# Performance work log

Measured on AMD Instinct MI355X. Metric: run time of the kernel, lower is better.

Reference implementation:

```python
import jax, jax.numpy as jnp
import numpy as np

B, T, IN_DIM = 128, 512, 32
H = 256            # h_dim; bidirectional -> embedding_dim D = 2*H = 512
N_EMB = 1024
BETA = 0.25


def setup_inputs() -> dict:
    key = jax.random.key(0)
    ks = jax.random.split(key, 12)
    traj = jax.random.normal(ks[0], (B, T, IN_DIM), dtype=jnp.float32)
    # variable-length padding mask: ones up to length, zeros after
    lengths = jax.random.randint(ks[1], (B,), 1, T + 1)
    mask = (jnp.arange(T)[None, :] < lengths[:, None]).astype(jnp.int32)
    s_x = 1.0 / np.sqrt(H)
    def u(k, shape):
        return jax.random.uniform(k, shape, jnp.float32, -s_x, s_x)
    # PyTorch GRU param layout: W_ih [3H, in], W_hh [3H, H], biases [3H]
    Wx_f, Wh_f = u(ks[2], (3 * H, IN_DIM)), u(ks[3], (3 * H, H))
    bx_f, bh_f = u(ks[4], (3 * H,)), u(ks[5], (3 * H,))
    Wx_b, Wh_b = u(ks[6], (3 * H, IN_DIM)), u(ks[7], (3 * H, H))
    bx_b, bh_b = u(ks[8], (3 * H,)), u(ks[9], (3 * H,))
    # codebook: nn.Embedding(n_embeddings, D) with uniform(-1/n, 1/n) init
    codebook = jax.random.uniform(ks[10], (N_EMB, 2 * H), jnp.float32,
                                  -1.0 / N_EMB, 1.0 / N_EMB)
    return {"traj": traj, "mask": mask,
            "Wx_f": Wx_f, "Wh_f": Wh_f, "bx_f": bx_f, "bh_f": bh_f,
            "Wx_b": Wx_b, "Wh_b": Wh_b, "bx_b": bx_b, "bh_b": bh_b,
            "codebook": codebook}


def _gru_dir(x, Wx, Wh, bx, bh):
    """Single-direction GRU over time (PyTorch gate math). x: [B,T,in] -> [B,T,H]."""
    b, t, _ = x.shape
    h_dim = Wh.shape[1]
    xg = jnp.einsum('bti,gi->btg', x, Wx) + bx  # precompute input gates [B,T,3H]
    def step(h, xg_t):
        hg = h @ Wh.T + bh
        xr, xz, xn = jnp.split(xg_t, 3, axis=-1)
        hr, hz, hn = jnp.split(hg, 3, axis=-1)
        r = jax.nn.sigmoid(xr + hr)
        z = jax.nn.sigmoid(xz + hz)
        n = jnp.tanh(xn + r * hn)
        h_new = (1.0 - z) * n + z * h
        return h_new, h_new
    h0 = jnp.zeros((b, h_dim), x.dtype)
    _, hs = jax.lax.scan(step, h0, jnp.swapaxes(xg, 0, 1))  # [T,B,H]
    return jnp.swapaxes(hs, 0, 1)


def _encode(traj, Wx_f, Wh_f, bx_f, bh_f, Wx_b, Wh_b, bx_b, bh_b):
    out_f = _gru_dir(traj, Wx_f, Wh_f, bx_f, bh_f)
    out_b = jnp.flip(_gru_dir(jnp.flip(traj, axis=1), Wx_b, Wh_b, bx_b, bh_b), axis=1)
    return jnp.concatenate([out_f, out_b], axis=-1)  # [B,T,2H]


def _vq(z_e, codebook, beta):
    # d(z, e) = |z|^2 + |e|^2 - 2 z.e  -> argmin over codebook
    d = (jnp.sum(z_e ** 2, axis=1, keepdims=True)
         + jnp.sum(codebook ** 2, axis=1)[None, :]
         - 2.0 * z_e @ codebook.T)                      # [B, N_EMB]
    idx = jnp.argmin(d, axis=1)                         # [B]
    z_q = codebook[idx]                                 # gather [B, D]
    loss = (jnp.mean((jax.lax.stop_gradient(z_q) - z_e) ** 2)
            + beta * jnp.mean((z_q - jax.lax.stop_gradient(z_e)) ** 2))
    z_q_st = z_e + jax.lax.stop_gradient(z_q - z_e)     # straight-through
    counts = jnp.zeros((codebook.shape[0],), z_e.dtype).at[idx].add(1.0)
    p = counts / z_e.shape[0]
    perplexity = jnp.exp(-jnp.sum(p * jnp.log(p + 1e-10)))
    return loss, z_q_st, perplexity, idx


def reference(traj, mask, Wx_f, Wh_f, bx_f, bh_f, Wx_b, Wh_b, bx_b, bh_b, codebook):
    z_e = _encode(traj, Wx_f, Wh_f, bx_f, bh_f, Wx_b, Wh_b, bx_b, bh_b)  # [B,T,2H]
    t = mask.shape[1]
    # last index where mask == 1:  T-1 - argmax(flip(mask))
    last_real_index = t - 1 - jnp.argmax(jnp.flip(mask, axis=1), axis=1)
    z_e_last = z_e[jnp.arange(z_e.shape[0]), last_real_index]            # [B,2H]
    loss, z_q, perplexity, _ = _vq(z_e_last, codebook, BETA)
    return z_q, loss, perplexity
```

## Files before the change

### kernel.cpp

```cpp
#include <hip/hip_runtime.h>
#include <math.h>

constexpr int B  = 128;
constexpr int T  = 512;
constexpr int IN = 32;
constexpr int H  = 256;
constexpr int D  = 2 * H;
constexpr int NC = 1024;

constexpr int NG   = 64;
constexpr int GW   = 4;
constexpr int SEQ  = 4;
constexpr int NTHR = 768;

constexpr int LDS_PAD_BYTES = 28672;


__global__ void k_zero(int* __restrict__ counts, double* __restrict__ lsum,
                       int* __restrict__ done,
                       unsigned long long* __restrict__ slab) {
    const int i = blockIdx.x * 256 + threadIdx.x;
    if (i < NC) counts[i] = 0;
    if (i == 0) { *lsum = 0.0; *done = 0; }
    slab[i] = 0ull;
}

__global__ void k_prep(const int* __restrict__ mask,
                       int* __restrict__ plan, int* __restrict__ slen,
                       int* __restrict__ glen) {
    __shared__ int ll[B];
    const int t = threadIdx.x;
    {
        const int b = t >> 2, q = t & 3;
        const int* mp = mask + b * T + q * 128;
        int s = 0;
        #pragma unroll
        for (int i = 0; i < 128; ++i) s += mp[i];
        s += __shfl_xor(s, 1, 64);
        s += __shfl_xor(s, 2, 64);
        if (q == 0) ll[b] = s - 1;
    }
    __syncthreads();
    if (t < B) {
        const int lf = ll[t] + 1;
        const int lb = T - ll[t];
        int rf = 0, rb = 0;
        for (int j = 0; j < B; ++j) {
            const int ljf = ll[j] + 1, ljb = T - ll[j];
            rf += (ljf > lf) || (ljf == lf && j < t);
            rb += (ljb > lb) || (ljb == lb && j < t);
        }
        plan[rf] = t;       slen[rf] = lf;
        plan[128 + rb] = t; slen[128 + rb] = lb;
        if ((rf & 3) == 0) glen[rf >> 2] = lf;
        if ((rb & 3) == 0) glen[32 + (rb >> 2)] = lb;
    }
}

__global__ void k_tc(float* __restrict__ cbT, const float* __restrict__ cb,
                     double* __restrict__ cbn2) {
    const int bid = blockIdx.x;
    if (bid < 512) {
        __shared__ float tile[32][33];
        const int tc = bid & 31;
        const int tk = bid >> 5;
        const int tx = threadIdx.x & 31, ty4 = threadIdx.x >> 5;
        #pragma unroll
        for (int j = 0; j < 4; ++j) {
            const int ty = ty4 * 4 + j;
            tile[ty][tx] = cb[(tc * 32 + ty) * D + tk * 32 + tx];
        }
        __syncthreads();
        #pragma unroll
        for (int j = 0; j < 4; ++j) {
            const int ty = ty4 * 4 + j;
            cbT[(tk * 32 + ty) * NC + tc * 32 + tx] = tile[tx][ty];
        }
    } else {
        const int c = (bid - 512) * 256 + threadIdx.x;
        double s = 0.0;
        for (int k = 0; k < D; ++k) {
            const double e = (double)cb[c * D + k];
            s += e * e;
        }
        cbn2[c] = s;
    }
}


__device__ __forceinline__ float sigmoidf_(float x) {
    return 1.0f / (1.0f + expf(-x));
}

__global__ __launch_bounds__(NTHR, 3) void k_gru(
    const float* __restrict__ traj,
    const float* __restrict__ Whf, const float* __restrict__ Whb,
    const float* __restrict__ Wxf, const float* __restrict__ Wxb,
    const float* __restrict__ bxf, const float* __restrict__ bhf,
    const float* __restrict__ bxb, const float* __restrict__ bhb,
    const int* __restrict__ plan, const int* __restrict__ slen,
    const int* __restrict__ glen,
    unsigned long long* __restrict__ hgt,
    float* __restrict__ ze)
{
    extern __shared__ float dynpad[];
    (void)dynpad;

    const int g   = blockIdx.x & 63;
    const int w   = blockIdx.x >> 6;
    const int dir = (g >= 32) ? 1 : 0;

    const float* __restrict__ Wh = dir ? Whb : Whf;
    const float* __restrict__ Wx = dir ? Wxb : Wxf;
    const float* __restrict__ bx = dir ? bxb : bxf;
    const float* __restrict__ bh = dir ? bhb : bhf;

    const int tid = threadIdx.x;
    const int kq  = tid / 96;
    const int rp  = tid - kq * 96;
    const int lr0 = 2 * rp;
    const int gi  = lr0 >> 6;
    const int Rg0 = gi * H + w * 64 + (lr0 & 63);

    __shared__ float4 h4[SEQ][64];
    __shared__ float  P [8][SEQ][194];
    __shared__ float  Px[8][SEQ][194];
    __shared__ float4 xb4[2][SEQ][8];
    __shared__ int    bbS[SEQ], lsS[SEQ];

    if (tid < SEQ) { bbS[tid] = plan[g * 4 + tid]; lsS[tid] = slen[g * 4 + tid]; }
    {
        float2* hp = (float2*)h4;
        if (tid < 512) hp[tid] = make_float2(0.0f, 0.0f);
    }
    const int L = glen[g];

    float4 wh[16];
    {
        const float4* p0 = (const float4*)(Wh + (size_t)Rg0 * 256 + kq * 32);
        const float4* p1 = (const float4*)(Wh + (size_t)(Rg0 + 1) * 256 + kq * 32);
        #pragma unroll
        for (int i = 0; i < 8; ++i) { wh[i] = p0[i]; wh[8 + i] = p1[i]; }
    }
    const float4 wx0 = *(const float4*)(Wx + Rg0 * 32 + kq * 4);
    const float4 wx1 = *(const float4*)(Wx + (Rg0 + 1) * 32 + kq * 4);

    float bxr = 0, bxz = 0, bxn = 0, bhr = 0, bhz = 0, bhn = 0;
    if (tid < 256) {
        const int j2 = tid & 63;
        bxr = bx[w * 64 + j2]; bxz = bx[H + w * 64 + j2]; bxn = bx[2 * H + w * 64 + j2];
        bhr = bh[w * 64 + j2]; bhz = bh[H + w * 64 + j2]; bhn = bh[2 * H + w * 64 + j2];
    }
    __syncthreads();
    if (tid < 128) {
        const int s = tid >> 5, i = tid & 31;
        const int t0 = dir ? (T - 1) : 0;
        ((float*)xb4)[128 + s * 32 + i] = traj[(bbS[s] * T + t0) * IN + i];
    }
    __syncthreads();

    const int u = tid - 256;

    for (int step = 1; step <= L; ++step) {
        const int buf = step & 1;
        unsigned long long* __restrict__ slab =
            hgt + (buf * NG + g) * (GW * SEQ * 64);

        float4 a0 = {0,0,0,0}, a1 = {0,0,0,0}, a2 = {0,0,0,0}, a3 = {0,0,0,0};
        float4 c0 = {0,0,0,0}, c1 = {0,0,0,0}, c2 = {0,0,0,0}, c3 = {0,0,0,0};
        #pragma unroll
        for (int i = 0; i < 8; ++i) {
            const float4 w0 = wh[i];
            const float4 w1 = wh[8 + i];
            float4 hv;
            hv = h4[0][kq * 8 + i];
            a0.x = fmaf(w0.x, hv.x, a0.x); a0.y = fmaf(w0.y, hv.y, a0.y);
            a0.z = fmaf(w0.z, hv.z, a0.z); a0.w = fmaf(w0.w, hv.w, a0.w);
            c0.x = fmaf(w1.x, hv.x, c0.x); c0.y = fmaf(w1.y, hv.y, c0.y);
            c0.z = fmaf(w1.z, hv.z, c0.z); c0.w = fmaf(w1.w, hv.w, c0.w);
            hv = h4[1][kq * 8 + i];
            a1.x = fmaf(w0.x, hv.x, a1.x); a1.y = fmaf(w0.y, hv.y, a1.y);
            a1.z = fmaf(w0.z, hv.z, a1.z); a1.w = fmaf(w0.w, hv.w, a1.w);
            c1.x = fmaf(w1.x, hv.x, c1.x); c1.y = fmaf(w1.y, hv.y, c1.y);
            c1.z = fmaf(w1.z, hv.z, c1.z); c1.w = fmaf(w1.w, hv.w, c1.w);
            hv = h4[2][kq * 8 + i];
            a2.x = fmaf(w0.x, hv.x, a2.x); a2.y = fmaf(w0.y, hv.y, a2.y);
            a2.z = fmaf(w0.z, hv.z, a2.z); a2.w = fmaf(w0.w, hv.w, a2.w);
            c2.x = fmaf(w1.x, hv.x, c2.x); c2.y = fmaf(w1.y, hv.y, c2.y);
            c2.z = fmaf(w1.z, hv.z, c2.z); c2.w = fmaf(w1.w, hv.w, c2.w);
            hv = h4[3][kq * 8 + i];
            a3.x = fmaf(w0.x, hv.x, a3.x); a3.y = fmaf(w0.y, hv.y, a3.y);
            a3.z = fmaf(w0.z, hv.z, a3.z); a3.w = fmaf(w0.w, hv.w, a3.w);
            c3.x = fmaf(w1.x, hv.x, c3.x); c3.y = fmaf(w1.y, hv.y, c3.y);
            c3.z = fmaf(w1.z, hv.z, c3.z); c3.w = fmaf(w1.w, hv.w, c3.w);
        }
        {
            float4 xv;
            float2 pv;
            xv = xb4[buf][0][kq];
            pv.x = a0.x + a0.y + a0.z + a0.w;
            pv.y = c0.x + c0.y + c0.z + c0.w;
            *(float2*)&P[kq][0][lr0] = pv;
            pv.x = wx0.x * xv.x + wx0.y * xv.y + wx0.z * xv.z + wx0.w * xv.w;
            pv.y = wx1.x * xv.x + wx1.y * xv.y + wx1.z * xv.z + wx1.w * xv.w;
            *(float2*)&Px[kq][0][lr0] = pv;
            xv = xb4[buf][1][kq];
            pv.x = a1.x + a1.y + a1.z + a1.w;
            pv.y = c1.x + c1.y + c1.z + c1.w;
            *(float2*)&P[kq][1][lr0] = pv;
            pv.x = wx0.x * xv.x + wx0.y * xv.y + wx0.z * xv.z + wx0.w * xv.w;
            pv.y = wx1.x * xv.x + wx1.y * xv.y + wx1.z * xv.z + wx1.w * xv.w;
            *(float2*)&Px[kq][1][lr0] = pv;
            xv = xb4[buf][2][kq];
            pv.x = a2.x + a2.y + a2.z + a2.w;
            pv.y = c2.x + c2.y + c2.z + c2.w;
            *(float2*)&P[kq][2][lr0] = pv;
            pv.x = wx0.x * xv.x + wx0.y * xv.y + wx0.z * xv.z + wx0.w * xv.w;
            pv.y = wx1.x * xv.x + wx1.y * xv.y + wx1.z * xv.z + wx1.w * xv.w;
            *(float2*)&Px[kq][2][lr0] = pv;
            xv = xb4[buf][3][kq];
            pv.x = a3.x + a3.y + a3.z + a3.w;
            pv.y = c3.x + c3.y + c3.z + c3.w;
            *(float2*)&P[kq][3][lr0] = pv;
            pv.x = wx0.x * xv.x + wx0.y * xv.y + wx0.z * xv.z + wx0.w * xv.w;
            pv.y = wx1.x * xv.x + wx1.y * xv.y + wx1.z * xv.z + wx1.w * xv.w;
            *(float2*)&Px[kq][3][lr0] = pv;
        }
        __syncthreads();

        if (tid < 256) {
            float xval = 0.0f;
            int xs = 0, xi = 0;
            const bool do_x = (tid < 128) && (step < L);
            if (do_x) {
                xs = tid >> 5; xi = tid & 31;
                const int tn = dir ? (T - 1 - step) : step;
                xval = traj[(bbS[xs] * T + tn) * IN + xi];
            }
            const int j2 = tid & 63, s = tid >> 6;
            float hr = 0.f, hz = 0.f, hn_ = 0.f, xr = 0.f, xz = 0.f, xn = 0.f;
            #pragma unroll
            for (int kk = 0; kk < 8; ++kk) {
                hr  += P [kk][s][j2];
                hz  += P [kk][s][64 + j2];
                hn_ += P [kk][s][128 + j2];
                xr  += Px[kk][s][j2];
                xz  += Px[kk][s][64 + j2];
                xn  += Px[kk][s][128 + j2];
            }
            const float r = sigmoidf_(xr + bxr + hr + bhr);
            const float z = sigmoidf_(xz + bxz + hz + bhz);
            const float n = tanhf(xn + bxn + r * (hn_ + bhn));
            const int jg = w * 64 + j2;
            const float hp = ((const float*)h4)[s * 256 + jg];
            const float hnew = (1.0f - z) * n + z * hp;
            ((float*)h4)[s * 256 + jg] = hnew;
            union { float f; unsigned ui; } cv; cv.f = hnew;
            const unsigned long long pk =
                ((unsigned long long)(unsigned)step << 32) | cv.ui;
            __hip_atomic_store(&slab[w * 256 + s * 64 + j2], pk,
                               __ATOMIC_RELAXED, __HIP_MEMORY_SCOPE_AGENT);
            if (step == lsS[s]) ze[bbS[s] * D + dir * H + jg] = hnew;
            const int pw0 = (0 >= w) ? 1 : 0;
            unsigned long long* ad0 = &slab[pw0 * 256 + s * 64 + j2];
            unsigned long long v0;
            do {
                v0 = __hip_atomic_load(ad0, __ATOMIC_RELAXED,
                                       __HIP_MEMORY_SCOPE_AGENT);
            } while ((int)(v0 >> 32) < step);
            union { unsigned ui; float f; } e0; e0.ui = (unsigned)v0;
            ((float*)h4)[s * 256 + pw0 * 64 + j2] = e0.f;
            if (do_x)
                ((float*)xb4)[(buf ^ 1) * 128 + xs * 32 + xi] = xval;
        } else {
            const int pi = 1 + (u >> 8);
            const int r2 = u & 255;
            const int s0 = r2 >> 6, j0 = r2 & 63;
            const int pw0 = pi + (pi >= w ? 1 : 0);
            unsigned long long* ad0 = &slab[pw0 * 256 + s0 * 64 + j0];
            unsigned long long v0;
            do {
                v0 = __hip_atomic_load(ad0, __ATOMIC_RELAXED,
                                       __HIP_MEMORY_SCOPE_AGENT);
            } while ((int)(v0 >> 32) < step);
            union { unsigned ui; float f; } e0; e0.ui = (unsigned)v0;
            ((float*)h4)[s0 * 256 + pw0 * 64 + j0] = e0.f;
        }
        __syncthreads();
    }
}


__global__ __launch_bounds__(256) void k_vq(
    const float* __restrict__ ze, const float* __restrict__ cbT,
    const float* __restrict__ cb, const double* __restrict__ cbn2,
    int* __restrict__ counts, double* __restrict__ lsum,
    int* __restrict__ done,
    float* __restrict__ out)
{
    __shared__ float lz[D];
    __shared__ double ds[256];
    __shared__ int cs[256];
    __shared__ int lastFlag;

    const int b = blockIdx.x;
    const int t = threadIdx.x;

    lz[t]       = ze[b * D + t];
    lz[t + 256] = ze[b * D + 256 + t];
    __syncthreads();

    double best = 1e300;
    int bc = 0;
    for (int m = 0; m < NC / 256; ++m) {
        const int c = m * 256 + t;
        double s2 = 0.0;
        #pragma unroll 4
        for (int k = 0; k < D; ++k)
            s2 += (double)lz[k] * (double)cbT[k * NC + c];
        const double dist = cbn2[c] - 2.0 * s2;
        if (dist < best) { best = dist; bc = c; }
    }
    ds[t] = best; cs[t] = bc;
    __syncthreads();
    for (int s = 128; s > 0; s >>= 1) {
        if (t < s) {
            if (ds[t + s] < ds[t] || (ds[t + s] == ds[t] && cs[t + s] < cs[t])) {
                ds[t] = ds[t + s]; cs[t] = cs[t + s];
            }
        }
        __syncthreads();
    }
    const int idx = cs[0];
    __syncthreads();

    if (t == 0) atomicAdd(&counts[idx], 1);

    double loc = 0.0;
    for (int jj = t; jj < D; jj += 256) {
        const float zev = lz[jj];
        const float zqv = cb[idx * D + jj];
        out[b * D + jj] = zev + (zqv - zev);
        const double df = (double)zqv - (double)zev;
        loc += df * df;
    }
    ds[t] = loc;
    __syncthreads();
    for (int s = 128; s > 0; s >>= 1) {
        if (t < s) ds[t] += ds[t + s];
        __syncthreads();
    }
    if (t == 0) atomicAdd(lsum, ds[0]);

    if (t == 0) {
        const int prev = __hip_atomic_fetch_add(done, 1, __ATOMIC_ACQ_REL,
                                                __HIP_MEMORY_SCOPE_AGENT);
        lastFlag = (prev == B - 1);
    }
    __syncthreads();
    if (lastFlag) {
        double s = 0.0;
        for (int c = t; c < NC; c += 256) {
            const int cnt = __hip_atomic_load(&counts[c], __ATOMIC_RELAXED,
                                              __HIP_MEMORY_SCOPE_AGENT);
            const double p = (double)cnt / (double)B;
            s += p * log(p + 1e-10);
        }
        ds[t] = s;
        __syncthreads();
        for (int r = 128; r > 0; r >>= 1) {
            if (t < r) ds[t] += ds[t + r];
            __syncthreads();
        }
        if (t == 0) {
            union { unsigned long long u; double d; } lv;
            lv.u = __hip_atomic_load((unsigned long long*)lsum,
                                     __ATOMIC_RELAXED, __HIP_MEMORY_SCOPE_AGENT);
            out[B * D]     = (float)(lv.d * 1.25 / (double)(B * D));
            out[B * D + 1] = (float)exp(-ds[0]);
        }
    }
}


extern "C" void kernel_launch(void* const* d_in, const int* in_sizes, int n_in,
                              void* d_out, int out_size, void* d_ws, size_t ws_size,
                              hipStream_t stream) {
    const float* traj = (const float*)d_in[0];
    const int*   mask = (const int*)d_in[1];
    const float* Wxf  = (const float*)d_in[2];
    const float* Whf  = (const float*)d_in[3];
    const float* bxf  = (const float*)d_in[4];
    const float* bhf  = (const float*)d_in[5];
    const float* Wxb  = (const float*)d_in[6];
    const float* Whb  = (const float*)d_in[7];
    const float* bxb  = (const float*)d_in[8];
    const float* bhb  = (const float*)d_in[9];
    const float* cb   = (const float*)d_in[10];
    float* out = (float*)d_out;

    float* ws    = (float*)d_ws;
    float* cbT   = ws;
    float* zebuf = cbT + 524288;
    unsigned long long* hgt =
        (unsigned long long*)(zebuf + 65536);
    int*   last  = (int*)(hgt + 131072);
    int*   plan  = last + 128;
    int*   slen  = plan + 256;
    int*   glen  = slen + 256;
    int*   cnts  = glen + 64;
    double* cbn2 = (double*)(cnts + 1024 + 4);
    double* lsum = cbn2 + 1024;
    int*   done  = (int*)(lsum + 1);

    k_zero<<<dim3(512), dim3(256), 0, stream>>>(cnts, lsum, done, hgt);
    k_prep<<<dim3(1), dim3(512), 0, stream>>>(mask, plan, slen, glen);
    k_tc  <<<dim3(516), dim3(256), 0, stream>>>(cbT, cb, cbn2);

    k_gru<<<dim3(NG * GW), dim3(NTHR), LDS_PAD_BYTES, stream>>>(
        traj, Whf, Whb, Wxf, Wxb, bxf, bhf, bxb, bhb,
        plan, slen, glen, hgt, zebuf);

    k_vq<<<dim3(B), dim3(256), 0, stream>>>(zebuf, cbT, cb, cbn2, cnts, lsum,
                                            done, out);
}
```

Before: 1.702 ms.

## Split GRU step into two sequence halves to overlap exchange with compute

Each recurrent step now processes the four sequences in two halves. The cross-workgroup hidden-state exchange for one half is waited on while the other half is being computed: the second half's previous-step values are polled after the first half's gates are computed, and vice versa. The aim is to hide inter-block spin-wait latency behind the matvec. The cost is twice as many block barriers per step and a more intricate slab-versioning scheme, which brings some risk of stalls or ordering bugs.

```diff
diff --git a/kernel.cpp b/kernel.cpp
--- a/kernel.cpp
+++ b/kernel.cpp
@@ -92,6 +92,10 @@
     return 1.0f / (1.0f + expf(-x));
 }
 
+#define FMA4(acc, wv, hv)                                                     \
+    acc.x = fmaf(wv.x, hv.x, acc.x); acc.y = fmaf(wv.y, hv.y, acc.y);         \
+    acc.z = fmaf(wv.z, hv.z, acc.z); acc.w = fmaf(wv.w, hv.w, acc.w);
+
 __global__ __launch_bounds__(NTHR, 3) void k_gru(
     const float* __restrict__ traj,
     const float* __restrict__ Whf, const float* __restrict__ Whb,
@@ -146,7 +150,7 @@
     const float4 wx1 = *(const float4*)(Wx + (Rg0 + 1) * 32 + kq * 4);
 
     float bxr = 0, bxz = 0, bxn = 0, bhr = 0, bhz = 0, bhn = 0;
-    if (tid < 256) {
+    if (tid < 128) {
         const int j2 = tid & 63;
         bxr = bx[w * 64 + j2]; bxz = bx[H + w * 64 + j2]; bxn = bx[2 * H + w * 64 + j2];
         bhr = bh[w * 64 + j2]; bhz = bh[H + w * 64 + j2]; bhn = bh[2 * H + w * 64 + j2];
@@ -159,44 +163,29 @@
     }
     __syncthreads();
 
-    const int u = tid - 256;
-
     for (int step = 1; step <= L; ++step) {
         const int buf = step & 1;
-        unsigned long long* __restrict__ slab =
+        unsigned long long* __restrict__ slabC =
             hgt + (buf * NG + g) * (GW * SEQ * 64);
-
-        float4 a0 = {0,0,0,0}, a1 = {0,0,0,0}, a2 = {0,0,0,0}, a3 = {0,0,0,0};
-        float4 c0 = {0,0,0,0}, c1 = {0,0,0,0}, c2 = {0,0,0,0}, c3 = {0,0,0,0};
-        #pragma unroll
-        for (int i = 0; i < 8; ++i) {
-            const float4 w0 = wh[i];
-            const float4 w1 = wh[8 + i];
-            float4 hv;
-            hv = h4[0][kq * 8 + i];
-            a0.x = fmaf(w0.x, hv.x, a0.x); a0.y = fmaf(w0.y, hv.y, a0.y);
-            a0.z = fmaf(w0.z, hv.z, a0.z); a0.w = fmaf(w0.w, hv.w, a0.w);
-            c0.x = fmaf(w1.x, hv.x, c0.x); c0.y = fmaf(w1.y, hv.y, c0.y);
-            c0.z = fmaf(w1.z, hv.z, c0.z); c0.w = fmaf(w1.w, hv.w, c0.w);
-            hv = h4[1][kq * 8 + i];
-            a1.x = fmaf(w0.x, hv.x, a1.x); a1.y = fmaf(w0.y, hv.y, a1.y);
-            a1.z = fmaf(w0.z, hv.z, a1.z); a1.w = fmaf(w0.w, hv.w, a1.w);
-            c1.x = fmaf(w1.x, hv.x, c1.x); c1.y = fmaf(w1.y, hv.y, c1.y);
-            c1.z = fmaf(w1.z, hv.z, c1.z); c1.w = fmaf(w1.w, hv.w, c1.w);
-            hv = h4[2][kq * 8 + i];
-            a2.x = fmaf(w0.x, hv.x, a2.x); a2.y = fmaf(w0.y, hv.y, a2.y);
-            a2.z = fmaf(w0.z, hv.z, a2.z); a2.w = fmaf(w0.w, hv.w, a2.w);
-            c2.x = fmaf(w1.x, hv.x, c2.x); c2.y = fmaf(w1.y, hv.y, c2.y);
-            c2.z = fmaf(w1.z, hv.z, c2.z); c2.w = fmaf(w1.w, hv.w, c2.w);
-            hv = h4[3][kq * 8 + i];
-            a3.x = fmaf(w0.x, hv.x, a3.x); a3.y = fmaf(w0.y, hv.y, a3.y);
-            a3.z = fmaf(w0.z, hv.z, a3.z); a3.w = fmaf(w0.w, hv.w, a3.w);
-            c3.x = fmaf(w1.x, hv.x, c3.x); c3.y = fmaf(w1.y, hv.y, c3.y);
-            c3.z = fmaf(w1.z, hv.z, c3.z); c3.w = fmaf(w1.w, hv.w, c3.w);
-        }
+        unsigned long long* __restrict__ slabP =
+            hgt + (((step - 1) & 1) * NG + g) * (GW * SEQ * 64);
+
+        float xval = 0.0f;
+
         {
-            float4 xv;
-            float2 pv;
+            float4 a0 = {0,0,0,0}, a1 = {0,0,0,0};
+            float4 c0 = {0,0,0,0}, c1 = {0,0,0,0};
+            #pragma unroll
+            for (int i = 0; i < 8; ++i) {
+                const float4 w0 = wh[i];
+                const float4 w1 = wh[8 + i];
+                float4 hv;
+                hv = h4[0][kq * 8 + i];
+                FMA4(a0, w0, hv); FMA4(c0, w1, hv);
+                hv = h4[1][kq * 8 + i];
+                FMA4(a1, w0, hv); FMA4(c1, w1, hv);
+            }
+            float4 xv; float2 pv;
             xv = xb4[buf][0][kq];
             pv.x = a0.x + a0.y + a0.z + a0.w;
             pv.y = c0.x + c0.y + c0.z + c0.w;
@@ -211,32 +200,10 @@
             pv.x = wx0.x * xv.x + wx0.y * xv.y + wx0.z * xv.z + wx0.w * xv.w;
             pv.y = wx1.x * xv.x + wx1.y * xv.y + wx1.z * xv.z + wx1.w * xv.w;
             *(float2*)&Px[kq][1][lr0] = pv;
-            xv = xb4[buf][2][kq];
-            pv.x = a2.x + a2.y + a2.z + a2.w;
-            pv.y = c2.x + c2.y + c2.z + c2.w;
-            *(float2*)&P[kq][2][lr0] = pv;
-            pv.x = wx0.x * xv.x + wx0.y * xv.y + wx0.z * xv.z + wx0.w * xv.w;
-            pv.y = wx1.x * xv.x + wx1.y * xv.y + wx1.z * xv.z + wx1.w * xv.w;
-            *(float2*)&Px[kq][2][lr0] = pv;
-            xv = xb4[buf][3][kq];
-            pv.x = a3.x + a3.y + a3.z + a3.w;
-            pv.y = c3.x + c3.y + c3.z + c3.w;
-            *(float2*)&P[kq][3][lr0] = pv;
-            pv.x = wx0.x * xv.x + wx0.y * xv.y + wx0.z * xv.z + wx0.w * xv.w;
-            pv.y = wx1.x * xv.x + wx1.y * xv.y + wx1.z * xv.z + wx1.w * xv.w;
-            *(float2*)&Px[kq][3][lr0] = pv;
-        }
-        __syncthreads();
-
-        if (tid < 256) {
-            float xval = 0.0f;
-            int xs = 0, xi = 0;
-            const bool do_x = (tid < 128) && (step < L);
-            if (do_x) {
-                xs = tid >> 5; xi = tid & 31;
-                const int tn = dir ? (T - 1 - step) : step;
-                xval = traj[(bbS[xs] * T + tn) * IN + xi];
-            }
+        }
+        __syncthreads();
+
+        if (tid < 128) {
             const int j2 = tid & 63, s = tid >> 6;
             float hr = 0.f, hz = 0.f, hn_ = 0.f, xr = 0.f, xz = 0.f, xn = 0.f;
             #pragma unroll
@@ -258,26 +225,97 @@
             union { float f; unsigned ui; } cv; cv.f = hnew;
             const unsigned long long pk =
                 ((unsigned long long)(unsigned)step << 32) | cv.ui;
-            __hip_atomic_store(&slab[w * 256 + s * 64 + j2], pk,
+            __hip_atomic_store(&slabC[w * 256 + s * 64 + j2], pk,
                                __ATOMIC_RELAXED, __HIP_MEMORY_SCOPE_AGENT);
             if (step == lsS[s]) ze[bbS[s] * D + dir * H + jg] = hnew;
-            const int pw0 = (0 >= w) ? 1 : 0;
-            unsigned long long* ad0 = &slab[pw0 * 256 + s * 64 + j2];
+        } else if (tid < 512) {
+            const int idx = tid - 128;
+            const int pi  = idx >> 7;
+            const int r2  = idx & 127;
+            const int s0  = 2 + (r2 >> 6), j0 = r2 & 63;
+            const int pw0 = pi + (pi >= w ? 1 : 0);
+            unsigned long long* ad0 = &slabP[pw0 * 256 + s0 * 64 + j0];
+            const int tg = step - 1;
             unsigned long long v0;
             do {
                 v0 = __hip_atomic_load(ad0, __ATOMIC_RELAXED,
                                        __HIP_MEMORY_SCOPE_AGENT);
-            } while ((int)(v0 >> 32) < step);
+            } while ((int)(v0 >> 32) < tg);
             union { unsigned ui; float f; } e0; e0.ui = (unsigned)v0;
-            ((float*)h4)[s * 256 + pw0 * 64 + j2] = e0.f;
-            if (do_x)
-                ((float*)xb4)[(buf ^ 1) * 128 + xs * 32 + xi] = xval;
-        } else {
-            const int pi = 1 + (u >> 8);
-            const int r2 = u & 255;
-            const int s0 = r2 >> 6, j0 = r2 & 63;
+            ((float*)h4)[s0 * 256 + pw0 * 64 + j0] = e0.f;
+        } else if (tid < 640) {
+            if (step < L) {
+                const int u2 = tid - 512;
+                const int xs = u2 >> 5, xi = u2 & 31;
+                const int tn = dir ? (T - 1 - step) : step;
+                xval = traj[(bbS[xs] * T + tn) * IN + xi];
+            }
+        }
+        __syncthreads();
+
+        {
+            float4 a0 = {0,0,0,0}, a1 = {0,0,0,0};
+            float4 c0 = {0,0,0,0}, c1 = {0,0,0,0};
+            #pragma unroll
+            for (int i = 0; i < 8; ++i) {
+                const float4 w0 = wh[i];
+                const float4 w1 = wh[8 + i];
+                float4 hv;
+                hv = h4[2][kq * 8 + i];
+                FMA4(a0, w0, hv); FMA4(c0, w1, hv);
+                hv = h4[3][kq * 8 + i];
+                FMA4(a1, w0, hv); FMA4(c1, w1, hv);
+            }
+            float4 xv; float2 pv;
+            xv = xb4[buf][2][kq];
+            pv.x = a0.x + a0.y + a0.z + a0.w;
+            pv.y = c0.x + c0.y + c0.z + c0.w;
+            *(float2*)&P[kq][2][lr0] = pv;
+            pv.x = wx0.x * xv.x + wx0.y * xv.y + wx0.z * xv.z + wx0.w * xv.w;
+            pv.y = wx1.x * xv.x + wx1.y * xv.y + wx1.z * xv.z + wx1.w * xv.w;
+            *(float2*)&Px[kq][2][lr0] = pv;
+            xv = xb4[buf][3][kq];
+            pv.x = a1.x + a1.y + a1.z + a1.w;
+            pv.y = c1.x + c1.y + c1.z + c1.w;
+            *(float2*)&P[kq][3][lr0] = pv;
+            pv.x = wx0.x * xv.x + wx0.y * xv.y + wx0.z * xv.z + wx0.w * xv.w;
+            pv.y = wx1.x * xv.x + wx1.y * xv.y + wx1.z * xv.z + wx1.w * xv.w;
+            *(float2*)&Px[kq][3][lr0] = pv;
+        }
+        __syncthreads();
+
+        if (tid < 128) {
+            const int j2 = tid & 63, s = 2 + (tid >> 6);
+            float hr = 0.f, hz = 0.f, hn_ = 0.f, xr = 0.f, xz = 0.f, xn = 0.f;
+            #pragma unroll
+            for (int kk = 0; kk < 8; ++kk) {
+                hr  += P [kk][s][j2];
+                hz  += P [kk][s][64 + j2];
+                hn_ += P [kk][s][128 + j2];
+                xr  += Px[kk][s][j2];
+                xz  += Px[kk][s][64 + j2];
+                xn  += Px[kk][s][128 + j2];
+            }
+            const float r = sigmoidf_(xr + bxr + hr + bhr);
+            const float z = sigmoidf_(xz + bxz + hz + bhz);
+            const float n = tanhf(xn + bxn + r * (hn_ + bhn));
+            const int jg = w * 64 + j2;
+            const float hp = ((const float*)h4)[s * 256 + jg];
+            const float hnew = (1.0f - z) * n + z * hp;
+            ((float*)h4)[s * 256 + jg] = hnew;
+            union { float f; unsigned ui; } cv; cv.f = hnew;
+            const unsigned long long pk =
+                ((unsigned long long)(unsigned)step << 32) | cv.ui;
+            __hip_atomic_store(&slabC[w * 256 + s * 64 + j2], pk,
+                               __ATOMIC_RELAXED, __HIP_MEMORY_SCOPE_AGENT);
+            if (step == lsS[s]) ze[bbS[s] * D + dir * H + jg] = hnew;
+        } else if (tid < 512) {
+            const int idx = tid - 128;
+            const int pi  = idx >> 7;
+            const int r2  = idx & 127;
+            const int s0  = r2 >> 6, j0 = r2 & 63;
             const int pw0 = pi + (pi >= w ? 1 : 0);
-            unsigned long long* ad0 = &slab[pw0 * 256 + s0 * 64 + j0];
+            unsigned long long* ad0 = &slabC[pw0 * 256 + s0 * 64 + j0];
             unsigned long long v0;
             do {
                 v0 = __hip_atomic_load(ad0, __ATOMIC_RELAXED,
@@ -285,6 +323,12 @@
             } while ((int)(v0 >> 32) < step);
             union { unsigned ui; float f; } e0; e0.ui = (unsigned)v0;
             ((float*)h4)[s0 * 256 + pw0 * 64 + j0] = e0.f;
+        } else if (tid < 640) {
+            if (step < L) {
+                const int u2 = tid - 512;
+                const int xs = u2 >> 5, xi = u2 & 31;
+                ((float*)xb4)[(buf ^ 1) * 128 + xs * 32 + xi] = xval;
+            }
         }
         __syncthreads();
     }
```

Result: slower. 3.875 ms (+127.7%).
